# Optimization experiments

Measured on AMD Instinct MI355X. Metric: run time of the kernel, lower is better.

## Reference

```python
import jax, jax.numpy as jnp
import numpy as np

D = 1024
B, S = 4, 2048
SCALE = D ** 0.5


def setup_inputs() -> dict:
    key = jax.random.key(0)
    k1, k2, k3 = jax.random.split(key, 3)
    x = jax.random.normal(k1, (B, S, D), dtype=jnp.float32)
    W_qkv = jax.random.normal(k2, (3 * D, D), dtype=jnp.float32) * (1.0 / np.sqrt(D))
    b_qkv = jax.random.normal(k3, (3 * D,), dtype=jnp.float32) * 0.01
    return {"x": x, "W_qkv": W_qkv, "b_qkv": b_qkv}


def reference(x, W_qkv, b_qkv):
    # nn.Linear: y = x @ W.T + b ; split into q, k, v along last dim
    qkv = jnp.einsum('bsd,ed->bse', x, W_qkv) + b_qkv  # [B, S, 3D]
    q, k, v = jnp.split(qkv, 3, axis=-1)
    scores = jnp.einsum('bqd,bkd->bqk', q, k) / SCALE  # [B, S, S]
    w = jax.nn.softmax(scores, axis=-1)
    out = jnp.einsum('bqk,bkd->bqd', w, v)             # [B, S, D]
    return (out, w)
```

## Files before the change

### kernel.cpp

```cpp
#include <hip/hip_runtime.h>
#include <math.h>


typedef unsigned short u16;
using bfrag = __attribute__((ext_vector_type(8))) short;
using f32x4 = __attribute__((ext_vector_type(4))) float;

#define BM 128
#define BN 128
#define BK 32

__device__ __forceinline__ unsigned pack_hi16(unsigned u0, unsigned u1) {
    return __builtin_amdgcn_perm(u1, u0, 0x07060302u);
}

__device__ __forceinline__ void split8(const float* f, unsigned* h, unsigned* l) {
    #pragma unroll
    for (int i = 0; i < 4; ++i) {
        const unsigned u0 = __float_as_uint(f[2 * i]);
        const unsigned u1 = __float_as_uint(f[2 * i + 1]);
        h[i] = pack_hi16(u0, u1);
        const float hf0 = __uint_as_float(u0 & 0xffff0000u);
        const float hf1 = __uint_as_float(u1 & 0xffff0000u);
        const unsigned v0 = __float_as_uint(f[2 * i] - hf0);
        const unsigned v1 = __float_as_uint(f[2 * i + 1] - hf1);
        l[i] = pack_hi16(v0, v1);
    }
}

__device__ __forceinline__ void g2lds16(const u16* g, short* l) {
    __builtin_amdgcn_global_load_lds(
        (const __attribute__((address_space(1))) void*)g,
        (__attribute__((address_space(3))) void*)l,
        16, 0, 0);
}

__device__ __forceinline__ void load_plane(
    const u16* __restrict__ g, long ld, short* l, int wave, int lane)
{
    #pragma unroll
    for (int t = 0; t < 2; ++t) {
        const int chunk = wave * 2 + t;
        const int row = chunk * 16 + (lane >> 2);
        const int g8 = ((lane & 3) ^ ((row >> 1) & 3)) << 3;
        g2lds16(g + (long)row * ld + g8, l + chunk * 512);
    }
}

__device__ __forceinline__ bfrag frag_ld(const short* plane, int row, int kg) {
    const int slot = kg ^ ((row >> 1) & 3);
    return *(const bfrag*)(plane + row * 32 + (slot << 3));
}

__global__ __launch_bounds__(256) void convert_split(
    const float* __restrict__ in, u16* __restrict__ hi, u16* __restrict__ lo,
    long n8)
{
    const long i = (long)blockIdx.x * blockDim.x + threadIdx.x;
    if (i >= n8) return;
    float f[8];
    *(float4*)&f[0] = ((const float4*)in)[i * 2];
    *(float4*)&f[4] = ((const float4*)in)[i * 2 + 1];
    unsigned h[4], l[4];
    split8(f, h, l);
    *(uint4*)&hi[i * 8] = make_uint4(h[0], h[1], h[2], h[3]);
    *(uint4*)&lo[i * 8] = make_uint4(l[0], l[1], l[2], l[3]);
}

__global__ __launch_bounds__(256) void transpose_v(
    const u16* __restrict__ vh, const u16* __restrict__ vl,
    u16* __restrict__ vTh, u16* __restrict__ vTl)
{
    __shared__ u16 tile[64][72];
    const u16* __restrict__ src = blockIdx.z ? vl : vh;
    u16* __restrict__ dst       = blockIdx.z ? vTl : vTh;

    const int d0 = blockIdx.x * 64;
    const int s0 = blockIdx.y * 64;
    const int t = threadIdx.x;
    const int r = t >> 2, cseg = (t & 3) * 16;

    *(uint4*)&tile[r][cseg]     = *(const uint4*)&src[(long)(s0 + r) * 1024 + d0 + cseg];
    *(uint4*)&tile[r][cseg + 8] = *(const uint4*)&src[(long)(s0 + r) * 1024 + d0 + cseg + 8];
    __syncthreads();

    u16 tmp[16];
    #pragma unroll
    for (int j = 0; j < 16; ++j) tmp[j] = tile[cseg + j][r];
    *(uint4*)&dst[(long)(d0 + r) * 8192 + s0 + cseg]     = *(uint4*)&tmp[0];
    *(uint4*)&dst[(long)(d0 + r) * 8192 + s0 + cseg + 8] = *(uint4*)&tmp[8];
}

template <int EPI>
__global__ __launch_bounds__(256) void gemm_planes(
    const u16* __restrict__ Ah_g, const u16* __restrict__ Al_g,
    const u16* __restrict__ Bh_g, const u16* __restrict__ Bl_g,
    const float* __restrict__ bias, float* __restrict__ C,
    u16* __restrict__ qh, u16* __restrict__ ql,
    u16* __restrict__ kh, u16* __restrict__ kl,
    u16* __restrict__ vh, u16* __restrict__ vl,
    int K, float scale, int lda, int ldb, int ldc,
    long bsA, long bsB, long bsC)
{
    Ah_g += (long)blockIdx.z * bsA;  Al_g += (long)blockIdx.z * bsA;
    Bh_g += (long)blockIdx.z * bsB;  Bl_g += (long)blockIdx.z * bsB;
    if (EPI == 0) C += (long)blockIdx.z * bsC;

    __shared__ __align__(16) short lds[4 * 4096];
    short* sAh = lds;
    short* sAl = lds + 4096;
    short* sBh = lds + 8192;
    short* sBl = lds + 12288;

    const int tid = threadIdx.x;
    const int lane = tid & 63;
    const int wave = tid >> 6;
    const int wr = wave >> 1, wc = wave & 1;

    const int row0 = blockIdx.y * BM;
    const int col0 = blockIdx.x * BN;

    f32x4 acc[4][4];
    const f32x4 fz = {0.f, 0.f, 0.f, 0.f};
    #pragma unroll
    for (int i = 0; i < 4; ++i)
        #pragma unroll
        for (int j = 0; j < 4; ++j) acc[i][j] = fz;

    const u16* At_h = Ah_g + (long)row0 * lda;
    const u16* At_l = Al_g + (long)row0 * lda;
    const u16* Bt_h = Bh_g + (long)col0 * ldb;
    const u16* Bt_l = Bl_g + (long)col0 * ldb;

    for (int k0 = 0; k0 < K; k0 += BK) {
        load_plane(At_h + k0, lda, sAh, wave, lane);
        load_plane(At_l + k0, lda, sAl, wave, lane);
        load_plane(Bt_h + k0, ldb, sBh, wave, lane);
        load_plane(Bt_l + k0, ldb, sBl, wave, lane);
        __syncthreads();

        const int kg = lane >> 4;
        const int arow = wr * 64 + (lane & 15);
        const int bcol = wc * 64 + (lane & 15);

        bfrag ah[4], al[4], bh[4], bl[4];
        #pragma unroll
        for (int mi = 0; mi < 4; ++mi) {
            ah[mi] = frag_ld(sAh, arow + mi * 16, kg);
            al[mi] = frag_ld(sAl, arow + mi * 16, kg);
        }
        #pragma unroll
        for (int nj = 0; nj < 4; ++nj) {
            bh[nj] = frag_ld(sBh, bcol + nj * 16, kg);
            bl[nj] = frag_ld(sBl, bcol + nj * 16, kg);
        }
        #pragma unroll
        for (int mi = 0; mi < 4; ++mi)
            #pragma unroll
            for (int nj = 0; nj < 4; ++nj) {
                acc[mi][nj] = __builtin_amdgcn_mfma_f32_16x16x32_bf16(
                    ah[mi], bh[nj], acc[mi][nj], 0, 0, 0);
                acc[mi][nj] = __builtin_amdgcn_mfma_f32_16x16x32_bf16(
                    ah[mi], bl[nj], acc[mi][nj], 0, 0, 0);
                acc[mi][nj] = __builtin_amdgcn_mfma_f32_16x16x32_bf16(
                    al[mi], bh[nj], acc[mi][nj], 0, 0, 0);
            }
        __syncthreads();
    }

    if (EPI == 0) {
        #pragma unroll
        for (int nj = 0; nj < 4; ++nj) {
            const int c = col0 + wc * 64 + nj * 16 + (lane & 15);
            #pragma unroll
            for (int mi = 0; mi < 4; ++mi) {
                const int rbase = row0 + wr * 64 + mi * 16 + (lane >> 4) * 4;
                #pragma unroll
                for (int r = 0; r < 4; ++r)
                    C[(long)(rbase + r) * ldc + c] = acc[mi][nj][r] * scale;
            }
        }
    } else {
        u16 *ph, *pl;
        int coff;
        if (col0 >= 2048)      { ph = vh; pl = vl; coff = 2048; }
        else if (col0 >= 1024) { ph = kh; pl = kl; coff = 1024; }
        else                   { ph = qh; pl = ql; coff = 0; }
        #pragma unroll
        for (int nj = 0; nj < 4; ++nj) {
            const int c = col0 + wc * 64 + nj * 16 + (lane & 15);
            const float bv = bias[c];
            const int cl = c - coff;
            #pragma unroll
            for (int mi = 0; mi < 4; ++mi) {
                const int rbase = row0 + wr * 64 + mi * 16 + (lane >> 4) * 4;
                #pragma unroll
                for (int r = 0; r < 4; ++r) {
                    const float val = acc[mi][nj][r] + bv;
                    const unsigned u = __float_as_uint(val);
                    const float fh = __uint_as_float(u & 0xffff0000u);
                    const long idx = (long)(rbase + r) * 1024 + cl;
                    ph[idx] = (u16)(u >> 16);
                    pl[idx] = (u16)(__float_as_uint(val - fh) >> 16);
                }
            }
        }
    }
}

__global__ __launch_bounds__(256) void gemm_wv(
    const float* __restrict__ A,
    const u16* __restrict__ Bh_g, const u16* __restrict__ Bl_g,
    float* __restrict__ C,
    int K, int lda, int ldb, int ldc, long bsA, long bsB, long bsC)
{
    A += (long)blockIdx.z * bsA;
    Bh_g += (long)blockIdx.z * bsB;  Bl_g += (long)blockIdx.z * bsB;
    C += (long)blockIdx.z * bsC;

    __shared__ __align__(16) short lds[4 * 4096];
    short* sAh = lds;
    short* sAl = lds + 4096;
    short* sBh = lds + 8192;
    short* sBl = lds + 12288;

    const int tid = threadIdx.x;
    const int lane = tid & 63;
    const int wave = tid >> 6;
    const int wr = wave >> 1, wc = wave & 1;

    const int row0 = blockIdx.y * BM;
    const int col0 = blockIdx.x * BN;

    const int sr = tid & 127;
    const int skw = tid >> 7;
    const int kgw = skw * 2;
    const int ssw = (sr >> 1) & 3;

    f32x4 acc[4][4];
    const f32x4 fz = {0.f, 0.f, 0.f, 0.f};
    #pragma unroll
    for (int i = 0; i < 4; ++i)
        #pragma unroll
        for (int j = 0; j < 4; ++j) acc[i][j] = fz;

    const float* At = A + (long)(row0 + sr) * lda;
    const u16* Bt_h = Bh_g + (long)col0 * ldb;
    const u16* Bt_l = Bl_g + (long)col0 * ldb;

    for (int k0 = 0; k0 < K; k0 += BK) {
        load_plane(Bt_h + k0, ldb, sBh, wave, lane);
        load_plane(Bt_l + k0, ldb, sBl, wave, lane);
        {
            const float* src = At + k0 + skw * 16;
            float f[16];
            *(float4*)&f[0]  = *(const float4*)(src + 0);
            *(float4*)&f[4]  = *(const float4*)(src + 4);
            *(float4*)&f[8]  = *(const float4*)(src + 8);
            *(float4*)&f[12] = *(const float4*)(src + 12);
            unsigned h[8], l[8];
            split8(f, h, l);
            split8(f + 8, h + 4, l + 4);
            short* rh = sAh + sr * 32;
            short* rl = sAl + sr * 32;
            *(uint4*)(rh + (((kgw)     ^ ssw) << 3)) = make_uint4(h[0], h[1], h[2], h[3]);
            *(uint4*)(rh + (((kgw + 1) ^ ssw) << 3)) = make_uint4(h[4], h[5], h[6], h[7]);
            *(uint4*)(rl + (((kgw)     ^ ssw) << 3)) = make_uint4(l[0], l[1], l[2], l[3]);
            *(uint4*)(rl + (((kgw + 1) ^ ssw) << 3)) = make_uint4(l[4], l[5], l[6], l[7]);
        }
        __syncthreads();

        const int kg = lane >> 4;
        const int arow = wr * 64 + (lane & 15);
        const int bcol = wc * 64 + (lane & 15);

        bfrag ah[4], al[4], bh[4], bl[4];
        #pragma unroll
        for (int mi = 0; mi < 4; ++mi) {
            ah[mi] = frag_ld(sAh, arow + mi * 16, kg);
            al[mi] = frag_ld(sAl, arow + mi * 16, kg);
        }
        #pragma unroll
        for (int nj = 0; nj < 4; ++nj) {
            bh[nj] = frag_ld(sBh, bcol + nj * 16, kg);
            bl[nj] = frag_ld(sBl, bcol + nj * 16, kg);
        }
        #pragma unroll
        for (int mi = 0; mi < 4; ++mi)
            #pragma unroll
            for (int nj = 0; nj < 4; ++nj) {
                acc[mi][nj] = __builtin_amdgcn_mfma_f32_16x16x32_bf16(
                    ah[mi], bh[nj], acc[mi][nj], 0, 0, 0);
                acc[mi][nj] = __builtin_amdgcn_mfma_f32_16x16x32_bf16(
                    ah[mi], bl[nj], acc[mi][nj], 0, 0, 0);
                acc[mi][nj] = __builtin_amdgcn_mfma_f32_16x16x32_bf16(
                    al[mi], bh[nj], acc[mi][nj], 0, 0, 0);
            }
        __syncthreads();
    }

    #pragma unroll
    for (int nj = 0; nj < 4; ++nj) {
        const int c = col0 + wc * 64 + nj * 16 + (lane & 15);
        #pragma unroll
        for (int mi = 0; mi < 4; ++mi) {
            const int rbase = row0 + wr * 64 + mi * 16 + (lane >> 4) * 4;
            #pragma unroll
            for (int r = 0; r < 4; ++r)
                C[(long)(rbase + r) * ldc + c] = acc[mi][nj][r];
        }
    }
}

__global__ __launch_bounds__(256) void softmax_kernel(float* __restrict__ w)
{
    const long row = blockIdx.x;
    float* p = w + row * 2048;
    const int tid = threadIdx.x;

    float v[8];
    float m = -INFINITY;
    #pragma unroll
    for (int i = 0; i < 8; ++i) {
        v[i] = p[tid + i * 256];
        m = fmaxf(m, v[i]);
    }
    #pragma unroll
    for (int off = 32; off > 0; off >>= 1)
        m = fmaxf(m, __shfl_xor(m, off));

    __shared__ float redm[4];
    __shared__ float reds[4];
    const int wave = tid >> 6;
    if ((tid & 63) == 0) redm[wave] = m;
    __syncthreads();
    m = fmaxf(fmaxf(redm[0], redm[1]), fmaxf(redm[2], redm[3]));

    float s = 0.f;
    #pragma unroll
    for (int i = 0; i < 8; ++i) {
        v[i] = __expf(v[i] - m);
        s += v[i];
    }
    #pragma unroll
    for (int off = 32; off > 0; off >>= 1)
        s += __shfl_xor(s, off);
    if ((tid & 63) == 0) reds[wave] = s;
    __syncthreads();
    s = reds[0] + reds[1] + reds[2] + reds[3];

    const float inv = 1.0f / s;
    #pragma unroll
    for (int i = 0; i < 8; ++i)
        p[tid + i * 256] = v[i] * inv;
}

extern "C" void kernel_launch(void* const* d_in, const int* in_sizes, int n_in,
                              void* d_out, int out_size, void* d_ws, size_t ws_size,
                              hipStream_t stream)
{
    constexpr int B = 4, S = 2048, D = 1024;
    constexpr long BS = (long)B * S;
    constexpr long P = BS * D;

    const float* x  = (const float*)d_in[0];
    const float* W  = (const float*)d_in[1];
    const float* bq = (const float*)d_in[2];

    float* out = (float*)d_out;
    float* w   = out + P;

    u16* wsu = (u16*)d_ws;
    u16 *qh = wsu,       *ql = qh + P;
    u16 *kh = ql + P,    *kl = kh + P;
    u16 *vTh = kl + P,   *vTl = vTh + P;

    u16* wscr = (u16*)w;
    u16 *xh = wscr,      *xl = xh + P;
    u16 *Wh = xl + P,    *Wl = Wh + 3 * D * D;

    u16 *vh = (u16*)out, *vl = vh + P;

    convert_split<<<dim3((unsigned)(P / 8 / 256)), 256, 0, stream>>>(x, xh, xl, P / 8);
    convert_split<<<dim3((unsigned)(3 * D * D / 8 / 256)), 256, 0, stream>>>(
        W, Wh, Wl, 3 * D * D / 8);

    gemm_planes<1><<<dim3(3 * D / BN, BS / BM, 1), 256, 0, stream>>>(
        xh, xl, Wh, Wl, bq, nullptr,
        qh, ql, kh, kl, vh, vl,
        D, 1.0f, D, D, 0, 0, 0, 0);

    transpose_v<<<dim3(D / 64, BS / 64, 2), 256, 0, stream>>>(vh, vl, vTh, vTl);

    gemm_planes<0><<<dim3(S / BN, S / BM, B), 256, 0, stream>>>(
        qh, ql, kh, kl, nullptr, w,
        nullptr, nullptr, nullptr, nullptr, nullptr, nullptr,
        D, 1.0f / 32.0f, D, D, S,
        (long)S * D, (long)S * D, (long)S * S);

    softmax_kernel<<<(int)BS, 256, 0, stream>>>(w);

    gemm_wv<<<dim3(D / BN, S / BM, B), 256, 0, stream>>>(
        w, vTh, vTl, out,
        S, S, (int)BS, D,
        (long)S * S, (long)S, (long)S * D);
}
```

Baseline: 549.5 us.

## Replace GEMMs with double-buffered 8-wave kernel and pre-split softmax output

Introduces a templated 512-thread GEMM that double-buffers LDS, staging the next K-tile's four planes interleaved with MFMA phases under setprio and sched barriers, and uses larger block tiles (up to 256x256). All three GEMMs use it. Softmax now also writes bf16 hi/lo planes of the weights into the workspace, so the W*V GEMM no longer splits fp32 on the fly. The goal is to hide global-to-LDS latency and raise data reuse. In exchange it uses more LDS and registers, adds workspace writes for the w planes (reusing the q/k region), and reads an extra plane pair instead of fp32 w.

After: 560.3 us. About the same (+2.0%).

```diff
diff --git a/kernel.cpp b/kernel.cpp
--- a/kernel.cpp
+++ b/kernel.cpp
@@ -5,10 +5,6 @@
 typedef unsigned short u16;
 using bfrag = __attribute__((ext_vector_type(8))) short;
 using f32x4 = __attribute__((ext_vector_type(4))) float;
-
-#define BM 128
-#define BN 128
-#define BK 32
 
 __device__ __forceinline__ unsigned pack_hi16(unsigned u0, unsigned u1) {
     return __builtin_amdgcn_perm(u1, u0, 0x07060302u);
@@ -35,12 +31,13 @@
         16, 0, 0);
 }
 
-__device__ __forceinline__ void load_plane(
+template <int ROWS>
+__device__ __forceinline__ void stage_plane(
     const u16* __restrict__ g, long ld, short* l, int wave, int lane)
 {
     #pragma unroll
-    for (int t = 0; t < 2; ++t) {
-        const int chunk = wave * 2 + t;
+    for (int t = 0; t < ROWS / 128; ++t) {
+        const int chunk = wave + t * 8;
         const int row = chunk * 16 + (lane >> 2);
         const int g8 = ((lane & 3) ^ ((row >> 1) & 3)) << 3;
         g2lds16(g + (long)row * ld + g8, l + chunk * 512);
@@ -50,6 +47,158 @@
 __device__ __forceinline__ bfrag frag_ld(const short* plane, int row, int kg) {
     const int slot = kg ^ ((row >> 1) & 3);
     return *(const bfrag*)(plane + row * 32 + (slot << 3));
+}
+
+template <int MREP, int NREP, int EPI>
+__global__ __launch_bounds__(512, 2) void gemm8(
+    const u16* __restrict__ Ah_g, const u16* __restrict__ Al_g,
+    const u16* __restrict__ Bh_g, const u16* __restrict__ Bl_g,
+    const float* __restrict__ bias, float* __restrict__ C,
+    u16* __restrict__ qh, u16* __restrict__ ql,
+    u16* __restrict__ kh, u16* __restrict__ kl,
+    u16* __restrict__ vh, u16* __restrict__ vl,
+    int K, float scale, int lda, int ldb, int ldc,
+    long bsA, long bsB, long bsC)
+{
+    constexpr int BMt = 2 * MREP * 16;
+    constexpr int BNt = 4 * NREP * 16;
+    constexpr int ASZ = BMt * 32;
+    constexpr int BSZ = BNt * 32;
+    constexpr int BUF = 2 * ASZ + 2 * BSZ;
+    constexpr int MI_PH = MREP / 4;
+
+    __shared__ __align__(16) short lds[2 * BUF];
+
+    Ah_g += (long)blockIdx.z * bsA;  Al_g += (long)blockIdx.z * bsA;
+    Bh_g += (long)blockIdx.z * bsB;  Bl_g += (long)blockIdx.z * bsB;
+    if (EPI == 0) C += (long)blockIdx.z * bsC;
+
+    const int tid  = threadIdx.x;
+    const int lane = tid & 63;
+    const int wave = tid >> 6;
+    const int wr = wave >> 2, wc = wave & 3;
+
+    const int row0 = blockIdx.y * BMt;
+    const int col0 = blockIdx.x * BNt;
+
+    const u16* At_h = Ah_g + (long)row0 * lda;
+    const u16* At_l = Al_g + (long)row0 * lda;
+    const u16* Bt_h = Bh_g + (long)col0 * ldb;
+    const u16* Bt_l = Bl_g + (long)col0 * ldb;
+
+    f32x4 acc[MREP][NREP];
+    const f32x4 fz = {0.f, 0.f, 0.f, 0.f};
+    #pragma unroll
+    for (int i = 0; i < MREP; ++i)
+        #pragma unroll
+        for (int j = 0; j < NREP; ++j) acc[i][j] = fz;
+
+    stage_plane<BMt>(At_h, lda, lds + 0,             wave, lane);
+    stage_plane<BMt>(At_l, lda, lds + ASZ,           wave, lane);
+    stage_plane<BNt>(Bt_h, ldb, lds + 2 * ASZ,       wave, lane);
+    stage_plane<BNt>(Bt_l, ldb, lds + 2 * ASZ + BSZ, wave, lane);
+    __syncthreads();
+
+    const int nt  = K / 32;
+    const int kg  = lane >> 4;
+    const int ar0 = wr * (MREP * 16) + (lane & 15);
+    const int bc0 = wc * (NREP * 16) + (lane & 15);
+    int cur = 0;
+
+    for (int t = 0; t < nt; ++t) {
+        const bool st = (t + 1 < nt);
+        short* base  = lds + cur * BUF;
+        short* nbase = lds + (cur ^ 1) * BUF;
+        const int k1 = (t + 1) * 32;
+        const short* sAh = base;
+        const short* sAl = base + ASZ;
+        const short* sBh = base + 2 * ASZ;
+        const short* sBl = base + 2 * ASZ + BSZ;
+
+        bfrag bh[NREP], bl[NREP];
+        #pragma unroll
+        for (int p = 0; p < 4; ++p) {
+            if (p == 0) {
+                #pragma unroll
+                for (int nj = 0; nj < NREP; ++nj) {
+                    bh[nj] = frag_ld(sBh, bc0 + nj * 16, kg);
+                    bl[nj] = frag_ld(sBl, bc0 + nj * 16, kg);
+                }
+            }
+            bfrag ah[MI_PH], al[MI_PH];
+            #pragma unroll
+            for (int q = 0; q < MI_PH; ++q) {
+                const int mi = p * MI_PH + q;
+                ah[q] = frag_ld(sAh, ar0 + mi * 16, kg);
+                al[q] = frag_ld(sAl, ar0 + mi * 16, kg);
+            }
+            if (st) {
+                if (p == 0) stage_plane<BMt>(At_h + k1, lda, nbase, wave, lane);
+                if (p == 1) stage_plane<BMt>(At_l + k1, lda, nbase + ASZ, wave, lane);
+                if (p == 2) stage_plane<BNt>(Bt_h + k1, ldb, nbase + 2 * ASZ, wave, lane);
+                if (p == 3) stage_plane<BNt>(Bt_l + k1, ldb, nbase + 2 * ASZ + BSZ, wave, lane);
+            }
+            __builtin_amdgcn_s_barrier();
+            __builtin_amdgcn_sched_barrier(0);
+            __builtin_amdgcn_s_setprio(1);
+            #pragma unroll
+            for (int q = 0; q < MI_PH; ++q) {
+                const int mi = p * MI_PH + q;
+                #pragma unroll
+                for (int nj = 0; nj < NREP; ++nj) {
+                    acc[mi][nj] = __builtin_amdgcn_mfma_f32_16x16x32_bf16(
+                        ah[q], bh[nj], acc[mi][nj], 0, 0, 0);
+                    acc[mi][nj] = __builtin_amdgcn_mfma_f32_16x16x32_bf16(
+                        ah[q], bl[nj], acc[mi][nj], 0, 0, 0);
+                    acc[mi][nj] = __builtin_amdgcn_mfma_f32_16x16x32_bf16(
+                        al[q], bh[nj], acc[mi][nj], 0, 0, 0);
+                }
+            }
+            __builtin_amdgcn_s_setprio(0);
+            __builtin_amdgcn_sched_barrier(0);
+            if (p < 3) __builtin_amdgcn_s_barrier();
+        }
+        if (st) { __syncthreads(); cur ^= 1; }
+    }
+
+    if (EPI == 0) {
+        #pragma unroll
+        for (int nj = 0; nj < NREP; ++nj) {
+            const int c = col0 + wc * (NREP * 16) + nj * 16 + (lane & 15);
+            #pragma unroll
+            for (int mi = 0; mi < MREP; ++mi) {
+                const int rb = row0 + wr * (MREP * 16) + mi * 16 + (lane >> 4) * 4;
+                #pragma unroll
+                for (int r = 0; r < 4; ++r)
+                    C[(long)(rb + r) * ldc + c] = acc[mi][nj][r] * scale;
+            }
+        }
+    } else {
+        u16 *ph, *pl;
+        int coff;
+        if (col0 >= 2048)      { ph = vh; pl = vl; coff = 2048; }
+        else if (col0 >= 1024) { ph = kh; pl = kl; coff = 1024; }
+        else                   { ph = qh; pl = ql; coff = 0; }
+        #pragma unroll
+        for (int nj = 0; nj < NREP; ++nj) {
+            const int c = col0 + wc * (NREP * 16) + nj * 16 + (lane & 15);
+            const float bv = bias[c];
+            const int cl = c - coff;
+            #pragma unroll
+            for (int mi = 0; mi < MREP; ++mi) {
+                const int rb = row0 + wr * (MREP * 16) + mi * 16 + (lane >> 4) * 4;
+                #pragma unroll
+                for (int r = 0; r < 4; ++r) {
+                    const float val = acc[mi][nj][r] + bv;
+                    const unsigned u = __float_as_uint(val);
+                    const float fh = __uint_as_float(u & 0xffff0000u);
+                    const long idx = (long)(rb + r) * 1024 + cl;
+                    ph[idx] = (u16)(u >> 16);
+                    pl[idx] = (u16)(__float_as_uint(val - fh) >> 16);
+                }
+            }
+        }
+    }
 }
 
 __global__ __launch_bounds__(256) void convert_split(
@@ -91,228 +240,8 @@
     *(uint4*)&dst[(long)(d0 + r) * 8192 + s0 + cseg + 8] = *(uint4*)&tmp[8];
 }
 
-template <int EPI>
-__global__ __launch_bounds__(256) void gemm_planes(
-    const u16* __restrict__ Ah_g, const u16* __restrict__ Al_g,
-    const u16* __restrict__ Bh_g, const u16* __restrict__ Bl_g,
-    const float* __restrict__ bias, float* __restrict__ C,
-    u16* __restrict__ qh, u16* __restrict__ ql,
-    u16* __restrict__ kh, u16* __restrict__ kl,
-    u16* __restrict__ vh, u16* __restrict__ vl,
-    int K, float scale, int lda, int ldb, int ldc,
-    long bsA, long bsB, long bsC)
-{
-    Ah_g += (long)blockIdx.z * bsA;  Al_g += (long)blockIdx.z * bsA;
-    Bh_g += (long)blockIdx.z * bsB;  Bl_g += (long)blockIdx.z * bsB;
-    if (EPI == 0) C += (long)blockIdx.z * bsC;
-
-    __shared__ __align__(16) short lds[4 * 4096];
-    short* sAh = lds;
-    short* sAl = lds + 4096;
-    short* sBh = lds + 8192;
-    short* sBl = lds + 12288;
-
-    const int tid = threadIdx.x;
-    const int lane = tid & 63;
-    const int wave = tid >> 6;
-    const int wr = wave >> 1, wc = wave & 1;
-
-    const int row0 = blockIdx.y * BM;
-    const int col0 = blockIdx.x * BN;
-
-    f32x4 acc[4][4];
-    const f32x4 fz = {0.f, 0.f, 0.f, 0.f};
-    #pragma unroll
-    for (int i = 0; i < 4; ++i)
-        #pragma unroll
-        for (int j = 0; j < 4; ++j) acc[i][j] = fz;
-
-    const u16* At_h = Ah_g + (long)row0 * lda;
-    const u16* At_l = Al_g + (long)row0 * lda;
-    const u16* Bt_h = Bh_g + (long)col0 * ldb;
-    const u16* Bt_l = Bl_g + (long)col0 * ldb;
-
-    for (int k0 = 0; k0 < K; k0 += BK) {
-        load_plane(At_h + k0, lda, sAh, wave, lane);
-        load_plane(At_l + k0, lda, sAl, wave, lane);
-        load_plane(Bt_h + k0, ldb, sBh, wave, lane);
-        load_plane(Bt_l + k0, ldb, sBl, wave, lane);
-        __syncthreads();
-
-        const int kg = lane >> 4;
-        const int arow = wr * 64 + (lane & 15);
-        const int bcol = wc * 64 + (lane & 15);
-
-        bfrag ah[4], al[4], bh[4], bl[4];
-        #pragma unroll
-        for (int mi = 0; mi < 4; ++mi) {
-            ah[mi] = frag_ld(sAh, arow + mi * 16, kg);
-            al[mi] = frag_ld(sAl, arow + mi * 16, kg);
-        }
-        #pragma unroll
-        for (int nj = 0; nj < 4; ++nj) {
-            bh[nj] = frag_ld(sBh, bcol + nj * 16, kg);
-            bl[nj] = frag_ld(sBl, bcol + nj * 16, kg);
-        }
-        #pragma unroll
-        for (int mi = 0; mi < 4; ++mi)
-            #pragma unroll
-            for (int nj = 0; nj < 4; ++nj) {
-                acc[mi][nj] = __builtin_amdgcn_mfma_f32_16x16x32_bf16(
-                    ah[mi], bh[nj], acc[mi][nj], 0, 0, 0);
-                acc[mi][nj] = __builtin_amdgcn_mfma_f32_16x16x32_bf16(
-                    ah[mi], bl[nj], acc[mi][nj], 0, 0, 0);
-                acc[mi][nj] = __builtin_amdgcn_mfma_f32_16x16x32_bf16(
-                    al[mi], bh[nj], acc[mi][nj], 0, 0, 0);
-            }
-        __syncthreads();
-    }
-
-    if (EPI == 0) {
-        #pragma unroll
-        for (int nj = 0; nj < 4; ++nj) {
-            const int c = col0 + wc * 64 + nj * 16 + (lane & 15);
-            #pragma unroll
-            for (int mi = 0; mi < 4; ++mi) {
-                const int rbase = row0 + wr * 64 + mi * 16 + (lane >> 4) * 4;
-                #pragma unroll
-                for (int r = 0; r < 4; ++r)
-                    C[(long)(rbase + r) * ldc + c] = acc[mi][nj][r] * scale;
-            }
-        }
-    } else {
-        u16 *ph, *pl;
-        int coff;
-        if (col0 >= 2048)      { ph = vh; pl = vl; coff = 2048; }
-        else if (col0 >= 1024) { ph = kh; pl = kl; coff = 1024; }
-        else                   { ph = qh; pl = ql; coff = 0; }
-        #pragma unroll
-        for (int nj = 0; nj < 4; ++nj) {
-            const int c = col0 + wc * 64 + nj * 16 + (lane & 15);
-            const float bv = bias[c];
-            const int cl = c - coff;
-            #pragma unroll
-            for (int mi = 0; mi < 4; ++mi) {
-                const int rbase = row0 + wr * 64 + mi * 16 + (lane >> 4) * 4;
-                #pragma unroll
-                for (int r = 0; r < 4; ++r) {
-                    const float val = acc[mi][nj][r] + bv;
-                    const unsigned u = __float_as_uint(val);
-                    const float fh = __uint_as_float(u & 0xffff0000u);
-                    const long idx = (long)(rbase + r) * 1024 + cl;
-                    ph[idx] = (u16)(u >> 16);
-                    pl[idx] = (u16)(__float_as_uint(val - fh) >> 16);
-                }
-            }
-        }
-    }
-}
-
-__global__ __launch_bounds__(256) void gemm_wv(
-    const float* __restrict__ A,
-    const u16* __restrict__ Bh_g, const u16* __restrict__ Bl_g,
-    float* __restrict__ C,
-    int K, int lda, int ldb, int ldc, long bsA, long bsB, long bsC)
-{
-    A += (long)blockIdx.z * bsA;
-    Bh_g += (long)blockIdx.z * bsB;  Bl_g += (long)blockIdx.z * bsB;
-    C += (long)blockIdx.z * bsC;
-
-    __shared__ __align__(16) short lds[4 * 4096];
-    short* sAh = lds;
-    short* sAl = lds + 4096;
-    short* sBh = lds + 8192;
-    short* sBl = lds + 12288;
-
-    const int tid = threadIdx.x;
-    const int lane = tid & 63;
-    const int wave = tid >> 6;
-    const int wr = wave >> 1, wc = wave & 1;
-
-    const int row0 = blockIdx.y * BM;
-    const int col0 = blockIdx.x * BN;
-
-    const int sr = tid & 127;
-    const int skw = tid >> 7;
-    const int kgw = skw * 2;
-    const int ssw = (sr >> 1) & 3;
-
-    f32x4 acc[4][4];
-    const f32x4 fz = {0.f, 0.f, 0.f, 0.f};
-    #pragma unroll
-    for (int i = 0; i < 4; ++i)
-        #pragma unroll
-        for (int j = 0; j < 4; ++j) acc[i][j] = fz;
-
-    const float* At = A + (long)(row0 + sr) * lda;
-    const u16* Bt_h = Bh_g + (long)col0 * ldb;
-    const u16* Bt_l = Bl_g + (long)col0 * ldb;
-
-    for (int k0 = 0; k0 < K; k0 += BK) {
-        load_plane(Bt_h + k0, ldb, sBh, wave, lane);
-        load_plane(Bt_l + k0, ldb, sBl, wave, lane);
-        {
-            const float* src = At + k0 + skw * 16;
-            float f[16];
-            *(float4*)&f[0]  = *(const float4*)(src + 0);
-            *(float4*)&f[4]  = *(const float4*)(src + 4);
-            *(float4*)&f[8]  = *(const float4*)(src + 8);
-            *(float4*)&f[12] = *(const float4*)(src + 12);
-            unsigned h[8], l[8];
-            split8(f, h, l);
-            split8(f + 8, h + 4, l + 4);
-            short* rh = sAh + sr * 32;
-            short* rl = sAl + sr * 32;
-            *(uint4*)(rh + (((kgw)     ^ ssw) << 3)) = make_uint4(h[0], h[1], h[2], h[3]);
-            *(uint4*)(rh + (((kgw + 1) ^ ssw) << 3)) = make_uint4(h[4], h[5], h[6], h[7]);
-            *(uint4*)(rl + (((kgw)     ^ ssw) << 3)) = make_uint4(l[0], l[1], l[2], l[3]);
-            *(uint4*)(rl + (((kgw + 1) ^ ssw) << 3)) = make_uint4(l[4], l[5], l[6], l[7]);
-        }
-        __syncthreads();
-
-        const int kg = lane >> 4;
-        const int arow = wr * 64 + (lane & 15);
-        const int bcol = wc * 64 + (lane & 15);
-
-        bfrag ah[4], al[4], bh[4], bl[4];
-        #pragma unroll
-        for (int mi = 0; mi < 4; ++mi) {
-            ah[mi] = frag_ld(sAh, arow + mi * 16, kg);
-            al[mi] = frag_ld(sAl, arow + mi * 16, kg);
-        }
-        #pragma unroll
-        for (int nj = 0; nj < 4; ++nj) {
-            bh[nj] = frag_ld(sBh, bcol + nj * 16, kg);
-            bl[nj] = frag_ld(sBl, bcol + nj * 16, kg);
-        }
-        #pragma unroll
-        for (int mi = 0; mi < 4; ++mi)
-            #pragma unroll
-            for (int nj = 0; nj < 4; ++nj) {
-                acc[mi][nj] = __builtin_amdgcn_mfma_f32_16x16x32_bf16(
-                    ah[mi], bh[nj], acc[mi][nj], 0, 0, 0);
-                acc[mi][nj] = __builtin_amdgcn_mfma_f32_16x16x32_bf16(
-                    ah[mi], bl[nj], acc[mi][nj], 0, 0, 0);
-                acc[mi][nj] = __builtin_amdgcn_mfma_f32_16x16x32_bf16(
-                    al[mi], bh[nj], acc[mi][nj], 0, 0, 0);
-            }
-        __syncthreads();
-    }
-
-    #pragma unroll
-    for (int nj = 0; nj < 4; ++nj) {
-        const int c = col0 + wc * 64 + nj * 16 + (lane & 15);
-        #pragma unroll
-        for (int mi = 0; mi < 4; ++mi) {
-            const int rbase = row0 + wr * 64 + mi * 16 + (lane >> 4) * 4;
-            #pragma unroll
-            for (int r = 0; r < 4; ++r)
-                C[(long)(rbase + r) * ldc + c] = acc[mi][nj][r];
-        }
-    }
-}
-
-__global__ __launch_bounds__(256) void softmax_kernel(float* __restrict__ w)
+__global__ __launch_bounds__(256) void softmax_kernel(
+    float* __restrict__ w, u16* __restrict__ wh, u16* __restrict__ wl)
 {
     const long row = blockIdx.x;
     float* p = w + row * 2048;
@@ -351,8 +280,15 @@
 
     const float inv = 1.0f / s;
     #pragma unroll
-    for (int i = 0; i < 8; ++i)
-        p[tid + i * 256] = v[i] * inv;
+    for (int i = 0; i < 8; ++i) {
+        const float y = v[i] * inv;
+        const long idx = row * 2048 + tid + i * 256;
+        w[idx] = y;
+        const unsigned u = __float_as_uint(y);
+        const float fh = __uint_as_float(u & 0xffff0000u);
+        wh[idx] = (u16)(u >> 16);
+        wl[idx] = (u16)(__float_as_uint(y - fh) >> 16);
+    }
 }
 
 extern "C" void kernel_launch(void* const* d_in, const int* in_sizes, int n_in,
@@ -374,6 +310,7 @@
     u16 *qh = wsu,       *ql = qh + P;
     u16 *kh = ql + P,    *kl = kh + P;
     u16 *vTh = kl + P,   *vTl = vTh + P;
+    u16 *wh = wsu,       *wl = wsu + 2 * P;
 
     u16* wscr = (u16*)w;
     u16 *xh = wscr,      *xl = xh + P;
@@ -385,23 +322,24 @@
     convert_split<<<dim3((unsigned)(3 * D * D / 8 / 256)), 256, 0, stream>>>(
         W, Wh, Wl, 3 * D * D / 8);
 
-    gemm_planes<1><<<dim3(3 * D / BN, BS / BM, 1), 256, 0, stream>>>(
+    gemm8<4, 4, 1><<<dim3(3 * D / 256, BS / 128, 1), 512, 0, stream>>>(
         xh, xl, Wh, Wl, bq, nullptr,
         qh, ql, kh, kl, vh, vl,
         D, 1.0f, D, D, 0, 0, 0, 0);
 
     transpose_v<<<dim3(D / 64, BS / 64, 2), 256, 0, stream>>>(vh, vl, vTh, vTl);
 
-    gemm_planes<0><<<dim3(S / BN, S / BM, B), 256, 0, stream>>>(
+    gemm8<8, 4, 0><<<dim3(S / 256, S / 256, B), 512, 0, stream>>>(
         qh, ql, kh, kl, nullptr, w,
         nullptr, nullptr, nullptr, nullptr, nullptr, nullptr,
         D, 1.0f / 32.0f, D, D, S,
         (long)S * D, (long)S * D, (long)S * S);
 
-    softmax_kernel<<<(int)BS, 256, 0, stream>>>(w);
-
-    gemm_wv<<<dim3(D / BN, S / BM, B), 256, 0, stream>>>(
-        w, vTh, vTl, out,
-        S, S, (int)BS, D,
+    softmax_kernel<<<(int)BS, 256, 0, stream>>>(w, wh, wl);
+
+    gemm8<8, 2, 0><<<dim3(D / 128, S / 256, B), 512, 0, stream>>>(
+        wh, wl, vTh, vTl, nullptr, out,
+        nullptr, nullptr, nullptr, nullptr, nullptr, nullptr,
+        S, 1.0f, S, (int)BS, D,
         (long)S * S, (long)S, (long)S * D);
 }
```
